# Performance work log

Hardware: AMD Instinct MI355X
Metric: run time of the kernel (lower is better)

## Reference

```python
import jax, jax.numpy as jnp
import numpy as np

LAYERS = 2
HIDDEN = 512
FFN = 2048
HEADS = 8
IMG = (32, 64)
SLEN = IMG[0] * IMG[1]
BSZ = 2
KEY_DIM = HIDDEN // HEADS      # 64
V_DIM = HIDDEN * 2             # 1024
HEAD_SIZE = V_DIM // HEADS     # 128
SCALE_BASE = 512.0
SCALING = KEY_DIM ** (-0.5)
LN_EPS = 1e-5


def xpos_apply(x):
    # x: [..., L, d]  (XPOS rotary with length-dependent decay, downscale=False)
    L, d = x.shape[-2], x.shape[-1]
    half = d // 2
    base = (jnp.arange(0, d, 2, dtype=jnp.float32) + 0.4 * d) / (1.4 * d)  # [half]
    min_pos = -(L // 2)
    pos = jnp.arange(min_pos, L + min_pos, dtype=jnp.float32)              # [L]
    scale = base[None, :] ** (pos[:, None] / SCALE_BASE)                   # [L, half]
    inv_freq = 1.0 / (10000.0 ** (jnp.arange(half, dtype=jnp.float32) / half))
    sinusoid = jnp.arange(L, dtype=jnp.float32)[:, None] * inv_freq[None, :]  # [L, half]
    sin = jnp.repeat(jnp.sin(sinusoid) * scale, 2, axis=-1)                # [L, d]
    cos = jnp.repeat(jnp.cos(sinusoid) * scale, 2, axis=-1)                # [L, d]
    x1 = x[..., 0::2]
    x2 = x[..., 1::2]
    rot = jnp.stack([-x2, x1], axis=-1).reshape(x.shape)  # rotate_every_two
    return x * cos + rot * sin


def layer_norm(x, g, b):
    mu = jnp.mean(x, axis=-1, keepdims=True)
    var = jnp.mean(jnp.square(x - mu), axis=-1, keepdims=True)
    return (x - mu) * jax.lax.rsqrt(var + LN_EPS) * g + b


def attention(x, Wq, Wk, Wv, Wo):
    B, S, _ = x.shape
    q = (x @ Wq).reshape(B, S, HEADS, KEY_DIM).transpose(0, 2, 1, 3)   # [B,H,S,dk]
    k = (x @ Wk).reshape(B, S, HEADS, KEY_DIM).transpose(0, 2, 1, 3)
    v = (x @ Wv).reshape(B, S, HEADS, HEAD_SIZE).transpose(0, 2, 1, 3)  # [B,H,S,hs]
    q = xpos_apply(q)
    k = xpos_apply(k)
    scores = jnp.einsum('bhqd,bhkd->bhqk', q, k)
    att = jax.nn.softmax(scores.astype(jnp.float32), axis=-1).astype(scores.dtype)
    att = att * SCALING  # note: scaling applied AFTER softmax, as in the source
    out = jnp.einsum('bhqk,bhkv->bhqv', att, v)                          # [B,H,S,hs]
    out = out.transpose(0, 2, 1, 3).reshape(B, S, V_DIM)
    return out @ Wo


def setup_inputs() -> dict:
    key = jax.random.key(0)
    ks = jax.random.split(key, 8)
    p = lambda k, shp: jax.random.normal(k, shp, dtype=jnp.float32) * 0.02
    return {
        'x':  jax.random.normal(ks[0], (BSZ, SLEN, HIDDEN), dtype=jnp.float32),
        'Wq': p(ks[1], (LAYERS, HIDDEN, HIDDEN)),
        'Wk': p(ks[2], (LAYERS, HIDDEN, HIDDEN)),
        'Wv': p(ks[3], (LAYERS, HIDDEN, V_DIM)),
        'Wo': p(ks[4], (LAYERS, V_DIM, HIDDEN)),
        'W1': p(ks[5], (LAYERS, HIDDEN, FFN)),
        'b1': jnp.zeros((LAYERS, FFN), jnp.float32),
        'W2': p(ks[6], (LAYERS, FFN, HIDDEN)),
        'b2': jnp.zeros((LAYERS, HIDDEN), jnp.float32),
        'g1': jnp.ones((LAYERS, HIDDEN), jnp.float32),
        'be1': jnp.zeros((LAYERS, HIDDEN), jnp.float32),
        'g2': jnp.ones((LAYERS, HIDDEN), jnp.float32),
        'be2': jnp.zeros((LAYERS, HIDDEN), jnp.float32),
    }


def reference(x, Wq, Wk, Wv, Wo, W1, b1, W2, b2, g1, be1, g2, be2):
    for i in range(LAYERS):
        y = layer_norm(x + attention(x, Wq[i], Wk[i], Wv[i], Wo[i]), g1[i], be1[i])
        ffn = jax.nn.relu(y @ W1[i] + b1[i]) @ W2[i] + b2[i]
        x = layer_norm(y + ffn, g2[i], be2[i])
    return x.reshape(x.shape[0], IMG[0], IMG[1], x.shape[2])
```

## Files before the change

### kernel.cpp

```cpp
#include <hip/hip_runtime.h>
#include <hip/hip_bf16.h>
#include <math.h>

#define LAYERS 2
#define HIDDEN 512
#define FFN_DIM 2048
#define HEADS 8
#define SLEN 2048
#define BSZ 2
#define MROWS 4096
#define ATT_SCALING 0.125f
#define LN_EPS 1e-5f
#define SCALE_BASE 512.0f
#define LOG2E 1.4426950408889634f

typedef unsigned short u16;
typedef unsigned int u32;
typedef __attribute__((ext_vector_type(8))) short bf16x8;
typedef __attribute__((ext_vector_type(4))) float f32x4;
typedef __attribute__((ext_vector_type(16))) float f32x16;

__device__ __forceinline__ float bf2f(u16 u) {
    union { u32 i; float f; } v; v.i = ((u32)u) << 16; return v.f;
}
__device__ __forceinline__ u16 f2bf(float f) {
    union { float f; u32 i; } v; v.f = f;
    u32 r = v.i + 0x7FFFu + ((v.i >> 16) & 1u);
    return (u16)(r >> 16);
}
__device__ __forceinline__ u32 pk2bf(float a, float b) {
    union { __hip_bfloat162 h; u32 u; } v;
    v.h = __float22bfloat162_rn(make_float2(a, b));
    return v.u;
}
__device__ __forceinline__ u32 cvtpk(float a, float b) {
    u32 r;
    asm("v_cvt_pk_bf16_f32 %0, %1, %2" : "=v"(r) : "v"(a), "v"(b));
    return r;
}
__device__ __forceinline__ void async16(const void* g, void* l) {
    __builtin_amdgcn_global_load_lds((const __attribute__((address_space(1))) void*)g,
                                     (__attribute__((address_space(3))) void*)l, 16, 0, 0);
}

__global__ __launch_bounds__(256) void prep_kernel(const float* __restrict__ x,
                                                   const float* __restrict__ Wq,
                                                   const float* __restrict__ Wk,
                                                   const float* __restrict__ Wv,
                                                   const float* __restrict__ Wo,
                                                   const float* __restrict__ W1,
                                                   const float* __restrict__ W2,
                                                   char* __restrict__ w,
                                                   float* __restrict__ Af,
                                                   u16* __restrict__ Ab,
                                                   float2* __restrict__ tab) {
    const size_t MB1 = 1u << 20;
    const int bid = blockIdx.x;
    const int tid = threadIdx.x;
    __shared__ float t[32][33];

    if (bid < 7168) {
        int l = bid / 3584;
        int tt = bid % 3584;
        u16* WqkvT = (u16*)(w + 48 * MB1 + (size_t)l * 2 * MB1);
        u16* WoT   = (u16*)(w + 52 * MB1 + (size_t)l * 1 * MB1);
        u16* W1T   = (u16*)(w + 54 * MB1 + (size_t)l * 2 * MB1);
        u16* W2T   = (u16*)(w + 58 * MB1 + (size_t)l * 2 * MB1);
        const float* src; u16* dst; int K, N, tix;
        if (tt < 256)       { src = Wq + (size_t)l * 512 * 512;  dst = WqkvT;              K = 512;  N = 512;  tix = tt; }
        else if (tt < 512)  { src = Wk + (size_t)l * 512 * 512;  dst = WqkvT + 512 * 512;  K = 512;  N = 512;  tix = tt - 256; }
        else if (tt < 1024) { src = Wv + (size_t)l * 512 * 1024; dst = WqkvT + 1024 * 512; K = 512;  N = 1024; tix = tt - 512; }
        else if (tt < 1536) { src = Wo + (size_t)l * 1024 * 512; dst = WoT;                K = 1024; N = 512;  tix = tt - 1024; }
        else if (tt < 2560) { src = W1 + (size_t)l * 512 * 2048; dst = W1T;                K = 512;  N = 2048; tix = tt - 1536; }
        else                { src = W2 + (size_t)l * 2048 * 512; dst = W2T;                K = 2048; N = 512;  tix = tt - 2560; }
        int ntx = N >> 5;
        int n0 = (tix % ntx) * 32, k0 = (tix / ntx) * 32;
        int tx = tid & 31, ty = tid >> 5;
#pragma unroll
        for (int i = 0; i < 4; i++)
            t[ty + 8 * i][tx] = src[(size_t)(k0 + ty + 8 * i) * N + n0 + tx];
        __syncthreads();
#pragma unroll
        for (int i = 0; i < 4; i++)
            dst[(size_t)(n0 + ty + 8 * i) * K + k0 + tx] = f2bf(t[tx][ty + 8 * i]);
    } else if (bid < 9216) {
        int i = ((bid - 7168) * 256 + tid) * 4;
        float4 v = *(const float4*)(x + i);
        *(float4*)(Af + i) = v;
        uint2 p;
        p.x = pk2bf(v.x, v.y);
        p.y = pk2bf(v.z, v.w);
        *(uint2*)(Ab + i) = p;
    } else {
        int idx = (bid - 9216) * 256 + tid;
        int j = idx & 31;
        int s = idx >> 5;
        float base = (2.0f * j + 0.4f * 64.0f) / (1.4f * 64.0f);
        float pos = (float)(s - 1024);
        float scale = powf(base, pos / SCALE_BASE);
        float inv_freq = powf(10000.0f, -(float)j / 32.0f);
        float ang = (float)s * inv_freq;
        tab[idx] = make_float2(cosf(ang) * scale, sinf(ang) * scale);
    }
}

__global__ __launch_bounds__(256) void xpos_vtrans(u16* __restrict__ QKV,
                                                   const float2* __restrict__ tab,
                                                   u16* __restrict__ VT) {
    const int bid = blockIdx.x;
    const int tid = threadIdx.x;
    __shared__ u16 t[64][65];

    if (bid < 4096) {
        int idx = bid * 256 + tid;
        int j = idx & 31;
        int h = (idx >> 5) & 7;
        int s = (idx >> 8) & 2047;
        int b = idx >> 19;

        float2 cssn = tab[s * 32 + j];
        float cs = cssn.x, sn = cssn.y;

        size_t off = (size_t)(b * SLEN + s) * 2048 + h * 64 + 2 * j;
        u32* pq = (u32*)(QKV + off);
        u32* pk = (u32*)(QKV + off + 512);

        u32 qv = *pq;
        float q0 = bf2f((u16)(qv & 0xffff)), q1 = bf2f((u16)(qv >> 16));
        *pq = pk2bf((q0 * cs - q1 * sn) * LOG2E, (q1 * cs + q0 * sn) * LOG2E);

        u32 kv = *pk;
        float k0 = bf2f((u16)(kv & 0xffff)), k1 = bf2f((u16)(kv >> 16));
        *pk = pk2bf(k0 * cs - k1 * sn, k1 * cs + k0 * sn);
    } else {
        int v = bid - 4096;
        int bz = v & 15;
        int vy = (v >> 4) & 1;
        int sx = v >> 5;
        int b = bz >> 3, h = bz & 7;
        int s0 = sx * 64, v0 = vy * 64;
#pragma unroll
        for (int i = 0; i < 16; i++) {
            int e = tid + i * 256; int r = e >> 6, c = e & 63;
            t[r][c] = QKV[(size_t)(b * SLEN + s0 + r) * 2048 + 1024 + h * 128 + v0 + c];
        }
        __syncthreads();
#pragma unroll
        for (int i = 0; i < 16; i++) {
            int e = tid + i * 256; int r = e >> 6, c = e & 63;
            VT[(size_t)((b * 8 + h) * 128 + v0 + r) * 2048 + s0 + c] = t[c][r];
        }
    }
}

template <int BM, int BN, int BK, int WM, int OUTF32, int BIAS, int RELU, int NSPLIT>
__global__ __launch_bounds__(256) void gemm_mfma(const u16* __restrict__ A,
                                                 const u16* __restrict__ WT,
                                                 const float* __restrict__ bias,
                                                 void* __restrict__ C0,
                                                 void* __restrict__ C1,
                                                 int M, int N, int K) {
    constexpr int WN  = 4 / WM;
    constexpr int AM  = BM / (WM * 16);
    constexpr int AN  = BN / (WN * 16);
    constexpr int KO  = BK / 32;
    constexpr int AIT = BM * BK / 2048;
    constexpr int BIT = BN * BK / 2048;
    constexpr int KB8 = BK / 8;

    __shared__ u16 As[2][BM * BK];
    __shared__ u16 Bs[2][BN * BK];

    const int tid  = threadIdx.x;
    const int wave = tid >> 6;
    const int lane = tid & 63;
    const int quad = lane >> 4;
    const int l15  = lane & 15;
    const int wm = wave % WM;
    const int wn = wave / WM;

    const int tm = blockIdx.y * BM;
    const int tn = blockIdx.x * BN;
    const int z  = (NSPLIT > 1) ? blockIdx.z : 0;
    const int Ksub = K / NSPLIT;
    const int k0g  = z * Ksub;

    auto issue = [&](int kt, int buf) {
#pragma unroll
        for (int it = 0; it < AIT; it++) {
            int cid = it * 256 + tid;
            async16(A + (size_t)(tm + cid / KB8) * K + k0g + kt + (cid % KB8) * 8,
                    (char*)As[buf] + (it * 256 + wave * 64) * 16);
        }
#pragma unroll
        for (int it = 0; it < BIT; it++) {
            int cid = it * 256 + tid;
            async16(WT + (size_t)(tn + cid / KB8) * K + k0g + kt + (cid % KB8) * 8,
                    (char*)Bs[buf] + (it * 256 + wave * 64) * 16);
        }
    };

    f32x4 acc[AM][AN];
#pragma unroll
    for (int i = 0; i < AM; i++)
#pragma unroll
        for (int j = 0; j < AN; j++) acc[i][j] = (f32x4){0.f, 0.f, 0.f, 0.f};

    const int nk = Ksub / BK;
    issue(0, 0);

    for (int t = 0; t < nk; t++) {
        __syncthreads();
        if (t + 1 < nk) issue((t + 1) * BK, (t + 1) & 1);
        const int buf = t & 1;

        bf16x8 af[KO][AM], bfr[KO][AN];
#pragma unroll
        for (int ko = 0; ko < KO; ko++) {
#pragma unroll
            for (int i = 0; i < AM; i++)
                af[ko][i] = *(const bf16x8*)((const char*)As[buf] +
                    (((wm * (AM * 16) + i * 16 + l15) * KB8) + ko * 4 + quad) * 16);
#pragma unroll
            for (int j = 0; j < AN; j++)
                bfr[ko][j] = *(const bf16x8*)((const char*)Bs[buf] +
                    (((wn * (AN * 16) + j * 16 + l15) * KB8) + ko * 4 + quad) * 16);
        }
#pragma unroll
        for (int ko = 0; ko < KO; ko++)
#pragma unroll
            for (int i = 0; i < AM; i++)
#pragma unroll
                for (int j = 0; j < AN; j++)
                    acc[i][j] = __builtin_amdgcn_mfma_f32_16x16x32_bf16(
                        af[ko][i], bfr[ko][j], acc[i][j], 0, 0, 0);
    }

    void* Cout = (NSPLIT > 1 && z) ? C1 : C0;
#pragma unroll
    for (int i = 0; i < AM; i++) {
#pragma unroll
        for (int j = 0; j < AN; j++) {
            int col = tn + wn * (AN * 16) + j * 16 + l15;
            float bv = (BIAS && z == 0) ? bias[col] : 0.0f;
#pragma unroll
            for (int r = 0; r < 4; r++) {
                int row = tm + wm * (AM * 16) + i * 16 + quad * 4 + r;
                float v = acc[i][j][r] + bv;
                if (RELU) v = fmaxf(v, 0.0f);
                if (OUTF32) ((float*)Cout)[(size_t)row * N + col] = v;
                else        ((u16*)Cout)[(size_t)row * N + col] = f2bf(v);
            }
        }
    }
}

__global__ __launch_bounds__(256, 2) void flash_attn_mfma(const u16* __restrict__ QKV,
                                                          const u16* __restrict__ VT,
                                                          u16* __restrict__ OP0,
                                                          u16* __restrict__ OP1,
                                                          float2* __restrict__ ML) {
    const int h  = blockIdx.x;
    const int q0 = blockIdx.y * 128;
    const int bz = blockIdx.z;
    const int b  = bz >> 1;
    const int split = bz & 1;
    const int tid  = threadIdx.x;
    const int wave = tid >> 6;
    const int lane = tid & 63;
    const int l31  = lane & 31;
    const int hi   = lane >> 5;
    const int swz  = (l31 & 7) ^ ((l31 >> 3) << 1);

    __shared__ u16 Ks[2][64 * 64];
    __shared__ u16 Vs[2][128 * 64];

    const int kb0 = split * 1024;

    const u16* kp[2];
    const u16* vp[4];
#pragma unroll
    for (int it = 0; it < 2; it++) {
        int cid = it * 256 + tid;
        int row = cid >> 3;
        int lc  = (cid & 7) ^ (row & 7) ^ (((row >> 3) & 3) << 1);
        kp[it] = QKV + (size_t)(b * SLEN + kb0 + row) * 2048 + 512 + h * 64 + lc * 8;
    }
#pragma unroll
    for (int it = 0; it < 4; it++) {
        int cid = it * 256 + tid;
        int row = cid >> 3;
        int lc  = (cid & 7) ^ (row & 7) ^ (((row >> 3) & 3) << 1);
        vp[it] = VT + (size_t)((b * 8 + h) * 128 + row) * 2048 + kb0 + lc * 8;
    }

    auto issueKV = [&](int buf) {
#pragma unroll
        for (int it = 0; it < 2; it++) {
            async16(kp[it], (char*)Ks[buf] + (it * 256 + wave * 64) * 16);
            kp[it] += 64 * 2048;
        }
#pragma unroll
        for (int it = 0; it < 4; it++) {
            async16(vp[it], (char*)Vs[buf] + (it * 256 + wave * 64) * 16);
            vp[it] += 64;
        }
    };

    bf16x8 qf[4];
    {
        const u16* p = QKV + (size_t)(b * SLEN + q0 + wave * 32 + l31) * 2048 +
                       h * 64 + hi * 8;
#pragma unroll
        for (int dc = 0; dc < 4; dc++) qf[dc] = *(const bf16x8*)(p + dc * 16);
    }

    f32x16 o_acc[4];
#pragma unroll
    for (int rb = 0; rb < 4; rb++)
#pragma unroll
        for (int r = 0; r < 16; r++) o_acc[rb][r] = 0.f;
    float m = -1e30f;
    float l = 0.f;

    issueKV(0);

    for (int ti = 0; ti < 16; ti++) {
        __syncthreads();
        if (ti + 1 < 16) issueKV((ti + 1) & 1);
        const int buf = ti & 1;

        f32x16 st[2];
#pragma unroll
        for (int kb = 0; kb < 2; kb++)
#pragma unroll
            for (int r = 0; r < 16; r++) st[kb][r] = 0.f;
        __builtin_amdgcn_s_setprio(1);
#pragma unroll
        for (int dc = 0; dc < 4; dc++)
#pragma unroll
            for (int kb = 0; kb < 2; kb++) {
                bf16x8 kf = *(const bf16x8*)((const char*)Ks[buf] +
                    ((kb * 32 + l31) * 8 + ((dc * 2 + hi) ^ swz)) * 16);
                st[kb] = __builtin_amdgcn_mfma_f32_32x32x16_bf16(kf, qf[dc],
                                                                 st[kb], 0, 0, 0);
            }
        __builtin_amdgcn_s_setprio(0);

        float fm[16];
#pragma unroll
        for (int r = 0; r < 16; r++) fm[r] = fmaxf(st[0][r], st[1][r]);
#pragma unroll
        for (int s = 8; s > 0; s >>= 1)
#pragma unroll
            for (int r = 0; r < s; r++) fm[r] = fmaxf(fm[r], fm[r + s]);
        float mx = fmaxf(fm[0], __shfl_xor(fm[0], 32, 64));

        float mnew = fmaxf(m, mx);
        float alpha = exp2f(m - mnew);
        m = mnew;

        float s0 = 0.f, s1 = 0.f, s2 = 0.f, s3 = 0.f;
#pragma unroll
        for (int kb = 0; kb < 2; kb++)
#pragma unroll
            for (int r = 0; r < 16; r += 4) {
                float p0 = exp2f(st[kb][r + 0] - mnew);
                float p1 = exp2f(st[kb][r + 1] - mnew);
                float p2 = exp2f(st[kb][r + 2] - mnew);
                float p3 = exp2f(st[kb][r + 3] - mnew);
                st[kb][r + 0] = p0; st[kb][r + 1] = p1;
                st[kb][r + 2] = p2; st[kb][r + 3] = p3;
                s0 += p0; s1 += p1; s2 += p2; s3 += p3;
            }
        float ls = (s0 + s1) + (s2 + s3);
        ls += __shfl_xor(ls, 32, 64);
        l = l * alpha + ls;

#pragma unroll
        for (int rb = 0; rb < 4; rb++)
#pragma unroll
            for (int r = 0; r < 16; r++) o_acc[rb][r] *= alpha;

#pragma unroll
        for (int kc = 0; kc < 4; kc++) {
            const int kb = kc >> 1, o = (kc & 1) * 8;
            u32 a1 = cvtpk(st[kb][o + 0], st[kb][o + 1]);
            u32 b1 = cvtpk(st[kb][o + 4], st[kb][o + 5]);
            u32 a2 = cvtpk(st[kb][o + 2], st[kb][o + 3]);
            u32 b2 = cvtpk(st[kb][o + 6], st[kb][o + 7]);
            asm volatile("v_permlane32_swap_b32 %0, %1" : "+v"(a1), "+v"(b1));
            asm volatile("v_permlane32_swap_b32 %0, %1" : "+v"(a2), "+v"(b2));
            union { u32 u[4]; bf16x8 v; } pf;
            pf.u[0] = a1; pf.u[1] = a2; pf.u[2] = b1; pf.u[3] = b2;
            __builtin_amdgcn_s_setprio(1);
#pragma unroll
            for (int rb = 0; rb < 4; rb++) {
                bf16x8 vb = *(const bf16x8*)((const char*)Vs[buf] +
                    ((rb * 32 + l31) * 8 + ((kc * 2 + hi) ^ swz)) * 16);
                o_acc[rb] = __builtin_amdgcn_mfma_f32_32x32x16_bf16(vb, pf.v,
                                                                    o_acc[rb], 0, 0, 0);
            }
            __builtin_amdgcn_s_setprio(0);
        }
    }

    u16* OP = split ? OP1 : OP0;
    const int q = q0 + wave * 32 + l31;
    if (lane < 32)
        ML[((size_t)(split * 2 + b) * 8 + h) * 2048 + q] = make_float2(m, l);
    size_t rowbase = ((size_t)(b * SLEN + q)) * 1024 + h * 128;
#pragma unroll
    for (int rb = 0; rb < 4; rb++)
#pragma unroll
        for (int i = 0; i < 8; i++) {
            int v = rb * 32 + ((2 * i) & 3) + 8 * (i >> 1) + 4 * hi;
            *(u32*)(OP + rowbase + v) =
                pk2bf(o_acc[rb][2 * i], o_acc[rb][2 * i + 1]);
        }
}

__global__ __launch_bounds__(256) void attn_combine(const u16* __restrict__ P0,
                                                    const u16* __restrict__ P1,
                                                    const float2* __restrict__ ML,
                                                    u16* __restrict__ AT) {
    int idx = (blockIdx.x * 256 + threadIdx.x) * 8;
    int hv = idx & 1023;
    int row = idx >> 10;
    int h = hv >> 7;
    int b = row >> 11, q = row & 2047;
    float2 ml0 = ML[((size_t)(0 + b) * 8 + h) * 2048 + q];
    float2 ml1 = ML[((size_t)(2 + b) * 8 + h) * 2048 + q];
    float M = fmaxf(ml0.x, ml1.x);
    float w0 = exp2f(ml0.x - M), w1 = exp2f(ml1.x - M);
    float L = ml0.y * w0 + ml1.y * w1;
    float sc = ATT_SCALING / L;
    w0 *= sc; w1 *= sc;

    uint4 a = *(const uint4*)(P0 + idx);
    uint4 c = *(const uint4*)(P1 + idx);
    uint4 o;
    u32 au[4] = {a.x, a.y, a.z, a.w};
    u32 cu[4] = {c.x, c.y, c.z, c.w};
    u32 ou[4];
#pragma unroll
    for (int k = 0; k < 4; k++) {
        float r0 = bf2f((u16)(au[k] & 0xffff)) * w0 + bf2f((u16)(cu[k] & 0xffff)) * w1;
        float r1 = bf2f((u16)(au[k] >> 16)) * w0 + bf2f((u16)(cu[k] >> 16)) * w1;
        ou[k] = pk2bf(r0, r1);
    }
    o.x = ou[0]; o.y = ou[1]; o.z = ou[2]; o.w = ou[3];
    *(uint4*)(AT + idx) = o;
}

__global__ __launch_bounds__(256) void addln_kernel(const float* __restrict__ X,
                                                    const float* __restrict__ R0,
                                                    const float* __restrict__ R1,
                                                    const float* __restrict__ g,
                                                    const float* __restrict__ be,
                                                    float* __restrict__ dstf,
                                                    u16* __restrict__ dstb) {
    const int row = blockIdx.x;
    const int tid = threadIdx.x;
    __shared__ float red[256];
    size_t off = (size_t)row * HIDDEN + 2 * tid;
    float2 a  = *(const float2*)(X + off);
    float2 r0 = *(const float2*)(R0 + off);
    float2 r1 = *(const float2*)(R1 + off);
    float v0 = a.x + r0.x + r1.x;
    float v1 = a.y + r0.y + r1.y;
    red[tid] = v0 + v1;
    __syncthreads();
    for (int s = 128; s > 0; s >>= 1) { if (tid < s) red[tid] += red[tid + s]; __syncthreads(); }
    float mu = red[0] * (1.0f / HIDDEN);
    __syncthreads();
    float d0 = v0 - mu, d1 = v1 - mu;
    red[tid] = d0 * d0 + d1 * d1;
    __syncthreads();
    for (int s = 128; s > 0; s >>= 1) { if (tid < s) red[tid] += red[tid + s]; __syncthreads(); }
    float rstd = rsqrtf(red[0] * (1.0f / HIDDEN) + LN_EPS);
    float2 gg = *(const float2*)(g + 2 * tid);
    float2 bb = *(const float2*)(be + 2 * tid);
    float o0 = d0 * rstd * gg.x + bb.x;
    float o1 = d1 * rstd * gg.y + bb.y;
    *(float2*)(dstf + off) = make_float2(o0, o1);
    *(u32*)(dstb + off) = pk2bf(o0, o1);
}

extern "C" void kernel_launch(void* const* d_in, const int* in_sizes, int n_in,
                              void* d_out, int out_size, void* d_ws, size_t ws_size,
                              hipStream_t stream) {
    const float* x   = (const float*)d_in[0];
    const float* Wq  = (const float*)d_in[1];
    const float* Wk  = (const float*)d_in[2];
    const float* Wv  = (const float*)d_in[3];
    const float* Wo  = (const float*)d_in[4];
    const float* W1  = (const float*)d_in[5];
    const float* b1  = (const float*)d_in[6];
    const float* W2  = (const float*)d_in[7];
    const float* b2  = (const float*)d_in[8];
    const float* g1  = (const float*)d_in[9];
    const float* be1 = (const float*)d_in[10];
    const float* g2  = (const float*)d_in[11];
    const float* be2 = (const float*)d_in[12];
    float* out = (float*)d_out;

    const size_t MB = 1u << 20;
    char* w = (char*)d_ws;
    float*  R1f  = (float*)(w);
    float*  F2a  = (float*)(w);
    u16*    VTg  = (u16*)(w + 8 * MB);
    float*  Yf   = (float*)(w + 8 * MB);
    u16*    OP1  = (u16*)(w + 16 * MB);
    float*  PfA  = (float*)(w + 16 * MB);
    float*  F2b  = (float*)(w + 16 * MB);
    u16*    QKV  = (u16*)(w + 24 * MB);
    float*  PfB  = (float*)(w + 24 * MB);
    u16*    F1   = (u16*)(w + 24 * MB);
    u16*    A_bf = (u16*)(w + 40 * MB);
    u16*    OP0  = (u16*)(w + 40 * MB);
    u16*    AT   = (u16*)(w + 40 * MB);
    u16*    Y_bf = (u16*)(w + 40 * MB);
    float2* xtab = (float2*)(w + 62 * MB);
    float2* ML   = (float2*)(w + 62 * MB + 512 * 1024);

    prep_kernel<<<9472, 256, 0, stream>>>(x, Wq, Wk, Wv, Wo, W1, W2,
                                          w, R1f, A_bf, xtab);

    for (int l = 0; l < LAYERS; l++) {
        u16* WqkvT = (u16*)(w + 48 * MB + (size_t)l * 2 * MB);
        u16* WoT   = (u16*)(w + 52 * MB + (size_t)l * 1 * MB);
        u16* W1T   = (u16*)(w + 54 * MB + (size_t)l * 2 * MB);
        u16* W2T   = (u16*)(w + 58 * MB + (size_t)l * 2 * MB);
        const float* b1_l  = b1 + (size_t)l * FFN_DIM;
        const float* b2_l  = b2 + (size_t)l * HIDDEN;
        const float* g1_l  = g1 + (size_t)l * HIDDEN;
        const float* be1_l = be1 + (size_t)l * HIDDEN;
        const float* g2_l  = g2 + (size_t)l * HIDDEN;
        const float* be2_l = be2 + (size_t)l * HIDDEN;

        gemm_mfma<128, 128, 64, 2, 0, 0, 0, 1><<<dim3(16, 32), 256, 0, stream>>>(
            A_bf, WqkvT, nullptr, QKV, nullptr, MROWS, 2048, 512);

        xpos_vtrans<<<5120, 256, 0, stream>>>(QKV, xtab, VTg);

        flash_attn_mfma<<<dim3(8, 16, 4), 256, 0, stream>>>(QKV, VTg, OP0, OP1, ML);
        attn_combine<<<MROWS * 1024 / 2048, 256, 0, stream>>>(OP0, OP1, ML, AT);

        gemm_mfma<128, 64, 64, 2, 1, 0, 0, 2><<<dim3(8, 32, 2), 256, 0, stream>>>(
            AT, WoT, nullptr, PfA, PfB, MROWS, 512, 1024);

        addln_kernel<<<MROWS, 256, 0, stream>>>(R1f, PfA, PfB, g1_l, be1_l, Yf, Y_bf);

        gemm_mfma<128, 128, 64, 2, 0, 1, 1, 1><<<dim3(16, 32), 256, 0, stream>>>(
            Y_bf, W1T, b1_l, F1, nullptr, MROWS, 2048, 512);

        gemm_mfma<128, 64, 64, 2, 1, 1, 0, 2><<<dim3(8, 32, 2), 256, 0, stream>>>(
            F1, W2T, b2_l, F2a, F2b, MROWS, 512, 2048);

        float* dstf = (l == LAYERS - 1) ? out : R1f;
        addln_kernel<<<MROWS, 256, 0, stream>>>(Yf, F2a, F2b, g2_l, be2_l, dstf, A_bf);
    }
}
```

Measured before the change: 405.4 us.

## Split flash-attention keys three ways with log-sum-exp combine and reused QKV buffer

Flash attention now splits the key range into three chunks (11/11/10 tiles of 64 keys) rather than two. This raises the grid from 512 to 768 blocks to fill more compute units, and the launch-bounds occupancy hint goes from 2 to 3 blocks per unit. Each split normalizes its output in-kernel and stores a single log-sum-exp value, and the combine kernel merges three partials. The third partial is written into the unused V columns of the QKV buffer with a row stride of 2048, which relies on those columns not being read again after the V transpose.

New measurement: 404.3 us. No clear change (-0.3%).

```diff
diff --git a/kernel.cpp b/kernel.cpp
--- a/kernel.cpp
+++ b/kernel.cpp
@@ -255,16 +255,17 @@
     }
 }
 
-__global__ __launch_bounds__(256, 2) void flash_attn_mfma(const u16* __restrict__ QKV,
+__global__ __launch_bounds__(256, 3) void flash_attn_mfma(const u16* __restrict__ QKV,
                                                           const u16* __restrict__ VT,
                                                           u16* __restrict__ OP0,
                                                           u16* __restrict__ OP1,
-                                                          float2* __restrict__ ML) {
+                                                          u16* __restrict__ OP2,
+                                                          float* __restrict__ MLW) {
     const int h  = blockIdx.x;
     const int q0 = blockIdx.y * 128;
     const int bz = blockIdx.z;
-    const int b  = bz >> 1;
-    const int split = bz & 1;
+    const int b  = bz / 3;
+    const int split = bz - b * 3;
     const int tid  = threadIdx.x;
     const int wave = tid >> 6;
     const int lane = tid & 63;
@@ -275,7 +276,8 @@
     __shared__ u16 Ks[2][64 * 64];
     __shared__ u16 Vs[2][128 * 64];
 
-    const int kb0 = split * 1024;
+    const int tcnt = (split == 2) ? 10 : 11;
+    const int kb0  = split * 704;
 
     const u16* kp[2];
     const u16* vp[4];
@@ -325,9 +327,9 @@
 
     issueKV(0);
 
-    for (int ti = 0; ti < 16; ti++) {
+    for (int ti = 0; ti < tcnt; ti++) {
         __syncthreads();
-        if (ti + 1 < 16) issueKV((ti + 1) & 1);
+        if (ti + 1 < tcnt) issueKV((ti + 1) & 1);
         const int buf = ti & 1;
 
         f32x16 st[2];
@@ -405,48 +407,55 @@
         }
     }
 
-    u16* OP = split ? OP1 : OP0;
     const int q = q0 + wave * 32 + l31;
     if (lane < 32)
-        ML[((size_t)(split * 2 + b) * 8 + h) * 2048 + q] = make_float2(m, l);
-    size_t rowbase = ((size_t)(b * SLEN + q)) * 1024 + h * 128;
+        MLW[((size_t)(b * 3 + split) * 8 + h) * 2048 + q] = m + __log2f(l);
+    const float invl = 1.0f / l;
+    u16* OP = (split == 0) ? OP0 : ((split == 1) ? OP1 : OP2);
+    const size_t rstride = (split == 2) ? 2048 : 1024;
+    size_t rowbase = ((size_t)(b * SLEN + q)) * rstride + h * 128;
 #pragma unroll
     for (int rb = 0; rb < 4; rb++)
 #pragma unroll
         for (int i = 0; i < 8; i++) {
             int v = rb * 32 + ((2 * i) & 3) + 8 * (i >> 1) + 4 * hi;
             *(u32*)(OP + rowbase + v) =
-                pk2bf(o_acc[rb][2 * i], o_acc[rb][2 * i + 1]);
+                pk2bf(o_acc[rb][2 * i] * invl, o_acc[rb][2 * i + 1] * invl);
         }
 }
 
 __global__ __launch_bounds__(256) void attn_combine(const u16* __restrict__ P0,
                                                     const u16* __restrict__ P1,
-                                                    const float2* __restrict__ ML,
+                                                    const u16* __restrict__ P2,
+                                                    const float* __restrict__ MLW,
                                                     u16* __restrict__ AT) {
     int idx = (blockIdx.x * 256 + threadIdx.x) * 8;
-    int hv = idx & 1023;
+    int col = idx & 1023;
     int row = idx >> 10;
-    int h = hv >> 7;
+    int h = col >> 7;
     int b = row >> 11, q = row & 2047;
-    float2 ml0 = ML[((size_t)(0 + b) * 8 + h) * 2048 + q];
-    float2 ml1 = ML[((size_t)(2 + b) * 8 + h) * 2048 + q];
-    float M = fmaxf(ml0.x, ml1.x);
-    float w0 = exp2f(ml0.x - M), w1 = exp2f(ml1.x - M);
-    float L = ml0.y * w0 + ml1.y * w1;
-    float sc = ATT_SCALING / L;
-    w0 *= sc; w1 *= sc;
+    float g0 = MLW[((size_t)(b * 3 + 0) * 8 + h) * 2048 + q];
+    float g1 = MLW[((size_t)(b * 3 + 1) * 8 + h) * 2048 + q];
+    float g2 = MLW[((size_t)(b * 3 + 2) * 8 + h) * 2048 + q];
+    float M = fmaxf(g0, fmaxf(g1, g2));
+    float e0 = exp2f(g0 - M), e1 = exp2f(g1 - M), e2 = exp2f(g2 - M);
+    float norm = ATT_SCALING / (e0 + e1 + e2);
+    e0 *= norm; e1 *= norm; e2 *= norm;
 
     uint4 a = *(const uint4*)(P0 + idx);
     uint4 c = *(const uint4*)(P1 + idx);
+    uint4 d = *(const uint4*)(P2 + (size_t)row * 2048 + col);
     uint4 o;
     u32 au[4] = {a.x, a.y, a.z, a.w};
     u32 cu[4] = {c.x, c.y, c.z, c.w};
+    u32 du[4] = {d.x, d.y, d.z, d.w};
     u32 ou[4];
 #pragma unroll
     for (int k = 0; k < 4; k++) {
-        float r0 = bf2f((u16)(au[k] & 0xffff)) * w0 + bf2f((u16)(cu[k] & 0xffff)) * w1;
-        float r1 = bf2f((u16)(au[k] >> 16)) * w0 + bf2f((u16)(cu[k] >> 16)) * w1;
+        float r0 = bf2f((u16)(au[k] & 0xffff)) * e0 + bf2f((u16)(cu[k] & 0xffff)) * e1 +
+                   bf2f((u16)(du[k] & 0xffff)) * e2;
+        float r1 = bf2f((u16)(au[k] >> 16)) * e0 + bf2f((u16)(cu[k] >> 16)) * e1 +
+                   bf2f((u16)(du[k] >> 16)) * e2;
         ou[k] = pk2bf(r0, r1);
     }
     o.x = ou[0]; o.y = ou[1]; o.z = ou[2]; o.w = ou[3];
@@ -522,7 +531,8 @@
     u16*    AT   = (u16*)(w + 40 * MB);
     u16*    Y_bf = (u16*)(w + 40 * MB);
     float2* xtab = (float2*)(w + 62 * MB);
-    float2* ML   = (float2*)(w + 62 * MB + 512 * 1024);
+    float*  MLW  = (float*)(w + 62 * MB + 512 * 1024);
+    u16*    OP2  = QKV + 1024;
 
     prep_kernel<<<9472, 256, 0, stream>>>(x, Wq, Wk, Wv, Wo, W1, W2,
                                           w, R1f, A_bf, xtab);
@@ -544,8 +554,10 @@
 
         xpos_vtrans<<<5120, 256, 0, stream>>>(QKV, xtab, VTg);
 
-        flash_attn_mfma<<<dim3(8, 16, 4), 256, 0, stream>>>(QKV, VTg, OP0, OP1, ML);
-        attn_combine<<<MROWS * 1024 / 2048, 256, 0, stream>>>(OP0, OP1, ML, AT);
+        flash_attn_mfma<<<dim3(8, 16, 6), 256, 0, stream>>>(QKV, VTg, OP0, OP1,
+                                                            OP2, MLW);
+        attn_combine<<<MROWS * 1024 / 2048, 256, 0, stream>>>(OP0, OP1, OP2,
+                                                              MLW, AT);
 
         gemm_mfma<128, 64, 64, 2, 1, 0, 0, 2><<<dim3(8, 32, 2), 256, 0, stream>>>(
             AT, WoT, nullptr, PfA, PfB, MROWS, 512, 1024);
```
